# Optimization experiments

Measured on AMD Instinct MI355X. Metric: run time of the kernel, lower is better.

Reference implementation:

```python
import jax, jax.numpy as jnp
import numpy as np
from jax import lax

HEADS = 8
DIM_HEAD = 64
DIM = HEADS * DIM_HEAD  # 512


def _dwconv(x_nchw, w):
    # depthwise 3x3, stride 1, pad 1 (SAME), groups = channels
    return lax.conv_general_dilated(
        x_nchw, w, window_strides=(1, 1), padding='SAME',
        feature_group_count=x_nchw.shape[1],
        dimension_numbers=('NCHW', 'OIHW', 'NCHW'))


def setup_inputs() -> dict:
    key = jax.random.key(0)
    ks = jax.random.split(key, 9)
    b, h, w, c = 4, 256, 256, DIM
    s = 1.0 / np.sqrt(c)
    return {
        'x_in':    jax.random.normal(ks[0], (b, h, w, c), jnp.float32),
        'Wq':      jax.random.normal(ks[1], (c, DIM), jnp.float32) * s,
        'Wk':      jax.random.normal(ks[2], (c, DIM), jnp.float32) * s,
        'Wv':      jax.random.normal(ks[3], (c, DIM), jnp.float32) * s,
        'rescale': jnp.ones((HEADS, 1, 1), jnp.float32),
        'proj_w':  jax.random.normal(ks[4], (DIM, c), jnp.float32) * s,
        'proj_b':  jnp.zeros((c,), jnp.float32),
        'conv1_w': jax.random.normal(ks[5], (c, 1, 3, 3), jnp.float32) * (1.0 / 3.0),
        'conv2_w': jax.random.normal(ks[6], (c, 1, 3, 3), jnp.float32) * (1.0 / 3.0),
    }


def reference(x_in, Wq, Wk, Wv, rescale, proj_w, proj_b, conv1_w, conv2_w):
    b, h, w, c = x_in.shape
    n = h * w
    x = x_in.reshape(b, n, c)
    q_inp = x @ Wq  # [b, n, heads*d]
    k_inp = x @ Wk
    v_inp = x @ Wv

    def heads_dn(t):  # [b, n, heads*d] -> [b, heads, d, n]
        return t.reshape(b, n, HEADS, DIM_HEAD).transpose(0, 2, 3, 1)

    q = heads_dn(q_inp)
    k = heads_dn(k_inp)
    v = heads_dn(v_inp)

    # L2-normalize along token axis (F.normalize, eps=1e-12)
    qn = q / jnp.maximum(jnp.linalg.norm(q, axis=-1, keepdims=True), 1e-12)
    kn = k / jnp.maximum(jnp.linalg.norm(k, axis=-1, keepdims=True), 1e-12)

    # channel attention: [b, heads, d, d]
    attn = jnp.einsum('bhdn,bhen->bhde', kn, qn) * rescale
    attn = jax.nn.softmax(attn, axis=-1)
    xo = jnp.einsum('bhde,bhen->bhdn', attn, v)  # [b, heads, d, n]

    xo = xo.transpose(0, 3, 1, 2).reshape(b, n, HEADS * DIM_HEAD)
    out_c = (xo @ proj_w + proj_b).reshape(b, h, w, c)

    # depthwise conv positional embedding on v_inp
    vp = v_inp.reshape(b, h, w, c).transpose(0, 3, 1, 2)  # NCHW
    vp = _dwconv(vp, conv1_w)
    vp = jax.nn.gelu(vp, approximate=False)
    vp = _dwconv(vp, conv2_w)
    out_p = vp.transpose(0, 2, 3, 1)

    return out_c + out_p
```

## Files before the change

kernel.cpp:

```cpp
#include <hip/hip_runtime.h>
#include <math.h>

typedef unsigned short u16;
typedef unsigned int   u32;
typedef __attribute__((ext_vector_type(4))) float f32x4;
typedef __attribute__((ext_vector_type(8))) short bf16x8;
typedef __attribute__((ext_vector_type(8))) u16   u16x8;
typedef __attribute__((ext_vector_type(4))) u16   u16x4;

#define DEVI static __device__ __forceinline__

DEVI float bf2f(u16 a){ u32 u=((u32)a)<<16; float f; __builtin_memcpy(&f,&u,4); return f; }
DEVI u16 f2bf(float f){ u32 u; __builtin_memcpy(&u,&f,4); u=u+0x7fffu+((u>>16)&1u); return (u16)(u>>16); }

DEVI void gload16(const u16* src, u16* lds){
  __builtin_amdgcn_global_load_lds((const __attribute__((address_space(1))) u32*)src,
                                   (__attribute__((address_space(3))) u32*)lds, 16, 0, 0);
}

__global__ void k_wvt(const float* __restrict__ Wv, u16* __restrict__ WvT){
  int n = blockIdx.x;
  for (int k = threadIdx.x; k < 512; k += 256)
    WvT[(size_t)n*512 + k] = f2bf(Wv[(size_t)k*512 + n]);
}
__global__ void k_wrep(const float* __restrict__ w1, const float* __restrict__ w2, float* __restrict__ wt){
  int s = blockIdx.x/9, tap = blockIdx.x%9, c = threadIdx.x;
  const float* w = s ? w2 : w1;
  wt[(size_t)(s*9+tap)*512 + c] = w[(size_t)c*9 + tap];
}

__global__ __launch_bounds__(512) void k_gemm_v(const float* __restrict__ x, const u16* __restrict__ WvT,
                                                u16* __restrict__ v, u16* __restrict__ xbT){
  extern __shared__ __align__(16) u16 sm[];
  const int tid = threadIdx.x;
  const int l = tid & 63, w = tid >> 6;
  const long r0 = (long)blockIdx.x * 128;
  f32x4 acc[8][4] = {};

  const int arow = tid >> 2, ac = tid & 3;
  const float* xp = x + (r0 + arow)*512 + ac*8;
  f32x4 rAa, rAb;

  auto LOADA = [&](int kk){ rAa = *(const f32x4*)(xp + kk); rAb = *(const f32x4*)(xp + kk + 4); };
  auto WRITEA = [&](int buf){
    u16x8 o;
    o[0]=f2bf(rAa.x); o[1]=f2bf(rAa.y); o[2]=f2bf(rAa.z); o[3]=f2bf(rAa.w);
    o[4]=f2bf(rAb.x); o[5]=f2bf(rAb.y); o[6]=f2bf(rAb.z); o[7]=f2bf(rAb.w);
    *(u16x8*)&sm[buf*4096 + arow*32 + ((ac ^ ((arow>>1)&3))*8)] = o;
  };
  auto GLOADB = [&](int buf, int kk){
    #pragma unroll
    for (int i = 0; i < 4; ++i){
      int blkrow = w*64 + i*16;
      int r = blkrow + (l>>2);
      const u16* src = WvT + (size_t)r*512 + kk + (((l&3) ^ ((l>>3)&3))*8);
      gload16(src, &sm[8192 + buf*16384 + blkrow*32]);
    }
  };

  LOADA(0); WRITEA(0); LOADA(32); GLOADB(0, 0);
  __syncthreads();
  for (int t = 0; t < 16; ++t){
    const int cur = t & 1;
    if (t < 15){
      WRITEA(cur^1);
      if (t < 14) LOADA((t+2)*32);
      GLOADB(cur^1, (t+1)*32);
    }
    const u16* Al = sm + cur*4096;
    const u16* Bl = sm + 8192 + cur*16384;
    bf16x8 bfr[4];
    #pragma unroll
    for (int nf = 0; nf < 4; ++nf){
      int row = w*64 + nf*16 + (l&15);
      bfr[nf] = *(const bf16x8*)&Bl[row*32 + (((l>>4) ^ ((row>>1)&3))*8)];
    }
    #pragma unroll
    for (int mf = 0; mf < 8; ++mf){
      int row = mf*16 + (l&15);
      bf16x8 af = *(const bf16x8*)&Al[row*32 + (((l>>4) ^ ((row>>1)&3))*8)];
      #pragma unroll
      for (int nf = 0; nf < 4; ++nf)
        acc[mf][nf] = __builtin_amdgcn_mfma_f32_16x16x32_bf16(af, bfr[nf], acc[mf][nf], 0,0,0);
    }
    {
      int chloc = tid & 31, tg = tid >> 5;
      u16x8 o;
      #pragma unroll
      for (int j = 0; j < 8; ++j){
        int tok = tg*8 + j;
        o[j] = Al[tok*32 + (((chloc>>3) ^ ((tok>>1)&3))*8) + (chloc&7)];
      }
      *(u16x8*)(xbT + (size_t)(t*32 + chloc)*262144 + r0 + tg*8) = o;
    }
    __syncthreads();
  }
  #pragma unroll
  for (int mf = 0; mf < 8; ++mf)
    #pragma unroll
    for (int nf = 0; nf < 4; ++nf){
      int col = w*64 + nf*16 + (l&15);
      #pragma unroll
      for (int j = 0; j < 4; ++j){
        long row = r0 + mf*16 + (l>>4)*4 + j;
        v[(size_t)row*512 + col] = f2bf(acc[mf][nf][j]);
      }
    }
}

__global__ __launch_bounds__(1024, 4) void k_syrk(const u16* __restrict__ xbT, float* __restrict__ P){
  __shared__ __align__(16) u16 AL[256*64];
  __shared__ __align__(16) u16 BL[256*64];
  const int bid = blockIdx.x;
  const int cs = bid & 63, combo = (bid>>6)%3, b = bid/192;
  const int hA = (combo==2) ? 1 : 0;
  const int tid = threadIdx.x;
  const int l = tid & 63, w = tid>>6, wi = w>>2, wj = w&3;
  const long tokb0 = (long)b*65536 + (long)cs*1024;
  const u16* Bread = (combo==1) ? BL : AL;
  f32x4 acc[4][4] = {};
  for (int st = 0; st < 16; ++st){
    const long tokb = tokb0 + st*64;
    #pragma unroll
    for (int i = 0; i < 2; ++i){
      int blkrow = w*16 + i*8;
      int r = blkrow + (l>>3);
      const u16* src = xbT + (size_t)(hA*256 + r)*262144 + tokb + (((l&7) ^ ((l>>3)&7))*8);
      gload16(src, &AL[blkrow*64]);
    }
    if (combo == 1){
      #pragma unroll
      for (int i = 0; i < 2; ++i){
        int blkrow = w*16 + i*8;
        int r = blkrow + (l>>3);
        const u16* src = xbT + (size_t)(256 + r)*262144 + tokb + (((l&7) ^ ((l>>3)&7))*8);
        gload16(src, &BL[blkrow*64]);
      }
    }
    __syncthreads();
    #pragma unroll
    for (int ks = 0; ks < 2; ++ks){
      bf16x8 af[4], bfr[4];
      #pragma unroll
      for (int mf = 0; mf < 4; ++mf){
        int row = wi*64 + mf*16 + (l&15);
        af[mf] = *(const bf16x8*)&AL[row*64 + (((ks*4 + (l>>4)) ^ (row&7))*8)];
      }
      #pragma unroll
      for (int nf = 0; nf < 4; ++nf){
        int row = wj*64 + nf*16 + (l&15);
        bfr[nf] = *(const bf16x8*)&Bread[row*64 + (((ks*4 + (l>>4)) ^ (row&7))*8)];
      }
      #pragma unroll
      for (int mf = 0; mf < 4; ++mf)
        #pragma unroll
        for (int nf = 0; nf < 4; ++nf)
          acc[mf][nf] = __builtin_amdgcn_mfma_f32_16x16x32_bf16(af[mf], bfr[nf], acc[mf][nf], 0,0,0);
    }
    __syncthreads();
  }
  float* Pb = P + (size_t)bid*65536;
  #pragma unroll
  for (int mf = 0; mf < 4; ++mf)
    #pragma unroll
    for (int nf = 0; nf < 4; ++nf)
      #pragma unroll
      for (int j = 0; j < 4; ++j){
        int il = wi*64 + mf*16 + (l>>4)*4 + j;
        int jl = wj*64 + nf*16 + (l&15);
        Pb[il*256 + jl] = acc[mf][nf][j];
      }
}

__global__ void k_sred(const float* __restrict__ P, float* __restrict__ S){
  int bid = blockIdx.x;
  int il = bid & 255, combo = (bid>>8)%3, b = bid/768;
  int hi = (combo==2)?1:0, hj = (combo==0)?0:1;
  int jl = threadIdx.x;
  float s = 0.f;
  for (int cs = 0; cs < 64; ++cs)
    s += P[((size_t)(b*192 + combo*64 + cs))*65536 + il*256 + jl];
  int I = hi*256 + il, J = hj*256 + jl;
  S[((size_t)b*512 + I)*512 + J] = s;
  if (combo == 1) S[((size_t)b*512 + J)*512 + I] = s;
}

__global__ __launch_bounds__(256) void k_a1(const float* __restrict__ S, const float* __restrict__ Wq,
                                            const float* __restrict__ Wk, float* __restrict__ T, float* __restrict__ U){
  int bid = blockIdx.x;
  int b = bid>>6, rem = bid&63, which = rem>>5, rbase = (rem&31)*16;
  const float* W = which ? Wk : Wq;
  float* O = which ? U : T;
  int tid = threadIdx.x;
  int rg = tid>>6, c0 = (tid&63)*8;
  const float* Sr = S + (size_t)b*262144 + (size_t)(rbase + rg*4)*512;
  float acc[4][8] = {};
  for (int k = 0; k < 512; ++k){
    float s0 = Sr[k], s1 = Sr[512+k], s2 = Sr[1024+k], s3 = Sr[1536+k];
    f32x4 wa = *(const f32x4*)(W + (size_t)k*512 + c0);
    f32x4 wb = *(const f32x4*)(W + (size_t)k*512 + c0 + 4);
    #pragma unroll
    for (int j = 0; j < 4; ++j){
      acc[0][j]   += s0*wa[j]; acc[1][j]   += s1*wa[j]; acc[2][j]   += s2*wa[j]; acc[3][j]   += s3*wa[j];
      acc[0][4+j] += s0*wb[j]; acc[1][4+j] += s1*wb[j]; acc[2][4+j] += s2*wb[j]; acc[3][4+j] += s3*wb[j];
    }
  }
  float* Ob = O + (size_t)b*262144;
  #pragma unroll
  for (int i = 0; i < 4; ++i){
    f32x4 o0, o1;
    o0.x=acc[i][0]; o0.y=acc[i][1]; o0.z=acc[i][2]; o0.w=acc[i][3];
    o1.x=acc[i][4]; o1.y=acc[i][5]; o1.z=acc[i][6]; o1.w=acc[i][7];
    *(f32x4*)(Ob + (size_t)(rbase+rg*4+i)*512 + c0)     = o0;
    *(f32x4*)(Ob + (size_t)(rbase+rg*4+i)*512 + c0 + 4) = o1;
  }
}

__global__ void k_a2(const float* __restrict__ Wq, const float* __restrict__ Wk,
                     const float* __restrict__ T, const float* __restrict__ U,
                     float* __restrict__ G, float* __restrict__ q2, float* __restrict__ k2){
  int b = blockIdx.x>>3, h = blockIdx.x&7;
  int tid = threadIdx.x;
  int d0 = (tid>>4)*4, e0 = (tid&15)*4;
  const float* Tb = T + (size_t)b*262144;
  float acc[4][4] = {};
  for (int i = 0; i < 512; ++i){
    f32x4 wk = *(const f32x4*)(Wk + (size_t)i*512 + h*64 + d0);
    f32x4 tv = *(const f32x4*)(Tb + (size_t)i*512 + h*64 + e0);
    #pragma unroll
    for (int di = 0; di < 4; ++di)
      #pragma unroll
      for (int ej = 0; ej < 4; ++ej) acc[di][ej] += wk[di]*tv[ej];
  }
  float* Gb = G + ((size_t)(b*8+h))*4096;
  #pragma unroll
  for (int di = 0; di < 4; ++di)
    #pragma unroll
    for (int ej = 0; ej < 4; ++ej) Gb[(d0+di)*64 + e0+ej] = acc[di][ej];
  if (tid < 64){
    int e = tid; float a = 0.f;
    for (int j = 0; j < 512; ++j) a += Wq[(size_t)j*512 + h*64 + e] * Tb[(size_t)j*512 + h*64 + e];
    q2[b*512 + h*64 + e] = a;
  } else if (tid < 128){
    int d = tid - 64; float a = 0.f;
    const float* Ub = U + (size_t)b*262144;
    for (int j = 0; j < 512; ++j) a += Wk[(size_t)j*512 + h*64 + d] * Ub[(size_t)j*512 + h*64 + d];
    k2[b*512 + h*64 + d] = a;
  }
}

__global__ void k_a3(const float* __restrict__ G, const float* __restrict__ resc,
                     const float* __restrict__ q2, const float* __restrict__ k2, float* __restrict__ Aa){
  int b = blockIdx.x>>3, h = blockIdx.x&7;
  int d = threadIdx.x;
  const float* g = G + ((size_t)(b*8+h))*4096 + d*64;
  float kn = fmaxf(sqrtf(k2[b*512 + h*64 + d]), 1e-12f);
  float sc = resc[h] / kn;
  float m = -3.4e38f;
  for (int e = 0; e < 64; ++e){
    float qn = fmaxf(sqrtf(q2[b*512 + h*64 + e]), 1e-12f);
    m = fmaxf(m, g[e]*sc/qn);
  }
  float ssum = 0.f;
  for (int e = 0; e < 64; ++e){
    float qn = fmaxf(sqrtf(q2[b*512 + h*64 + e]), 1e-12f);
    ssum += expf(g[e]*sc/qn - m);
  }
  float inv = 1.0f/ssum;
  float* ao = Aa + ((size_t)(b*8+h))*4096 + d*64;
  for (int e = 0; e < 64; ++e){
    float qn = fmaxf(sqrtf(q2[b*512 + h*64 + e]), 1e-12f);
    ao[e] = expf(g[e]*sc/qn - m)*inv;
  }
}

__global__ void k_a4(const float* __restrict__ Aa, const float* __restrict__ pw, u16* __restrict__ MT){
  int bid = blockIdx.x;
  int jt = bid&3, h = (bid>>2)&7, b = bid>>5;
  int tid = threadIdx.x;
  int j = jt*128 + (tid&127), eh = tid>>7;
  const float* Ab = Aa + ((size_t)(b*8+h))*4096;
  float acc[32] = {};
  for (int d = 0; d < 64; ++d){
    float p = pw[(size_t)(h*64+d)*512 + j];
    const float* ar = Ab + d*64 + eh*32;
    #pragma unroll
    for (int q = 0; q < 8; ++q){
      f32x4 pa = *(const f32x4*)(ar + q*4);
      acc[q*4+0] += pa.x*p; acc[q*4+1] += pa.y*p; acc[q*4+2] += pa.z*p; acc[q*4+3] += pa.w*p;
    }
  }
  u16* mo = MT + (size_t)b*262144 + (size_t)j*512 + h*64 + eh*32;
  #pragma unroll
  for (int q = 0; q < 16; ++q){
    u32 pk = (u32)f2bf(acc[2*q]) | ((u32)f2bf(acc[2*q+1])<<16);
    *(u32*)&mo[2*q] = pk;
  }
}

__global__ __launch_bounds__(256) void k_conv_fused(const u16* __restrict__ v, const float* __restrict__ wt,
                                                    u16* __restrict__ cbuf){
  __shared__ float vtf[400*16];
  __shared__ float t1f[324*16];
  const int logical = (blockIdx.x & 7)*4096 + (blockIdx.x >> 3);
  const int g = logical & 31, tx = (logical>>5)&15, ty = (logical>>9)&15, b = logical>>13;
  const int c0 = g*16, oy0 = ty*16, ox0 = tx*16;
  const int tid = threadIdx.x;
  const int quad = tid & 3;

  for (int k = 0; k < 7; ++k){
    int q = tid + k*256; if (q >= 1600) break;
    int pos = q >> 2;
    int ly = pos / 20, lx = pos - ly*20;
    int gy = oy0 - 2 + ly, gx = ox0 - 2 + lx;
    f32x4 val = {};
    if (gy >= 0 && gy < 256 && gx >= 0 && gx < 256){
      u16x4 raw = *(const u16x4*)(v + ((size_t)(b*65536 + gy*256 + gx))*512 + c0 + quad*4);
      val.x = bf2f(raw[0]); val.y = bf2f(raw[1]); val.z = bf2f(raw[2]); val.w = bf2f(raw[3]);
    }
    *(f32x4*)&vtf[pos*16 + quad*4] = val;
  }

  f32x4 wq[9];
  #pragma unroll
  for (int tap = 0; tap < 9; ++tap)
    wq[tap] = *(const f32x4*)(wt + (size_t)tap*512 + c0 + quad*4);
  __syncthreads();

  for (int k = 0; k < 6; ++k){
    int q = tid + k*256; if (q >= 1296) break;
    int pos = q >> 2;
    int y1 = pos / 18, x1 = pos - y1*18;
    int gy1 = oy0 - 1 + y1, gx1 = ox0 - 1 + x1;
    bool inimg = (gy1 >= 0 && gy1 < 256 && gx1 >= 0 && gx1 < 256);
    const float* base = &vtf[(y1*20 + x1)*16 + quad*4];
    float acc[4] = {};
    #pragma unroll
    for (int tap = 0; tap < 9; ++tap){
      int dy = tap/3, dx = tap - dy*3;
      f32x4 vv = *(const f32x4*)(base + (dy*20 + dx)*16);
      #pragma unroll
      for (int j = 0; j < 4; ++j) acc[j] += vv[j]*wq[tap][j];
    }
    f32x4 o;
    #pragma unroll
    for (int j = 0; j < 4; ++j){
      float a = acc[j];
      float gl = a / (1.0f + __expf(-1.5957691216f*a*(1.0f + 0.044715f*a*a)));
      o[j] = inimg ? gl : 0.0f;
    }
    *(f32x4*)&t1f[pos*16 + quad*4] = o;
  }

  #pragma unroll
  for (int tap = 0; tap < 9; ++tap)
    wq[tap] = *(const f32x4*)(wt + (size_t)(9+tap)*512 + c0 + quad*4);
  __syncthreads();

  #pragma unroll
  for (int k = 0; k < 4; ++k){
    int q = tid + k*256;
    int pos = q >> 2;
    int y2 = pos >> 4, x2 = pos & 15;
    const float* base = &t1f[(y2*18 + x2)*16 + quad*4];
    float acc[4] = {};
    #pragma unroll
    for (int tap = 0; tap < 9; ++tap){
      int dy = tap/3, dx = tap - dy*3;
      f32x4 tt = *(const f32x4*)(base + (dy*18 + dx)*16);
      #pragma unroll
      for (int j = 0; j < 4; ++j) acc[j] += tt[j]*wq[tap][j];
    }
    u16x4 o;
    #pragma unroll
    for (int j = 0; j < 4; ++j) o[j] = f2bf(acc[j]);
    size_t tok = (size_t)b*65536 + (size_t)(oy0+y2)*256 + (ox0+x2);
    *(u16x4*)(cbuf + tok*512 + c0 + quad*4) = o;
  }
}

__global__ __launch_bounds__(512, 2) void k_gemm_out(const u16* __restrict__ v, const u16* __restrict__ MT,
                                                     const float* __restrict__ proj_b, const u16* __restrict__ cbuf,
                                                     float* __restrict__ out){
  extern __shared__ __align__(16) u16 sm[];
  const int tid = threadIdx.x;
  const int l = tid & 63, w = tid >> 6;
  const int wr = w >> 2, wc = w & 3;
  const int bid = blockIdx.x;
  const int wg = (bid & 7)*256 + (bid >> 3);
  const long r0 = (long)(wg >> 1) * 256;
  const int  c0b = (wg & 1) * 256;
  const int  b = (int)(r0 >> 16);
  const u16* Mb = MT + (size_t)b*262144;
  f32x4 acc[8][4] = {};

  auto STAGE = [&](int buf, int k0){
    u16* Ab = sm + buf*16384;
    u16* Bb = sm + 32768 + buf*16384;
    #pragma unroll
    for (int i = 0; i < 4; ++i){
      int blkrow = w*32 + i*8;
      int r = blkrow + (l>>3);
      gload16(v + (size_t)(r0 + r)*512 + k0 + (((l&7) ^ (r&7))*8), Ab + blkrow*64);
    }
    #pragma unroll
    for (int i = 0; i < 4; ++i){
      int blkrow = w*32 + i*8;
      int r = blkrow + (l>>3);
      gload16(Mb + (size_t)(c0b + r)*512 + k0 + (((l&7) ^ (r&7))*8), Bb + blkrow*64);
    }
  };

  STAGE(0, 0);
  __syncthreads();
  for (int t = 0; t < 8; ++t){
    const int cur = t & 1;
    if (t < 7) STAGE(cur^1, (t+1)*64);
    const u16* Al = sm + cur*16384;
    const u16* Bl = sm + 32768 + cur*16384;
    #pragma unroll
    for (int ks = 0; ks < 2; ++ks){
      bf16x8 bfr[4];
      #pragma unroll
      for (int nf = 0; nf < 4; ++nf){
        int row = wc*64 + nf*16 + (l&15);
        bfr[nf] = *(const bf16x8*)&Bl[row*64 + (((ks*4 + (l>>4)) ^ (row&7))*8)];
      }
      #pragma unroll
      for (int mf = 0; mf < 8; ++mf){
        int row = wr*128 + mf*16 + (l&15);
        bf16x8 af = *(const bf16x8*)&Al[row*64 + (((ks*4 + (l>>4)) ^ (row&7))*8)];
        #pragma unroll
        for (int nf = 0; nf < 4; ++nf)
          acc[mf][nf] = __builtin_amdgcn_mfma_f32_16x16x32_bf16(af, bfr[nf], acc[mf][nf], 0,0,0);
      }
    }
    __syncthreads();
  }
  #pragma unroll
  for (int mf = 0; mf < 8; ++mf)
    #pragma unroll
    for (int nf = 0; nf < 4; ++nf){
      int col = c0b + wc*64 + nf*16 + (l&15);
      float pb = proj_b[col];
      #pragma unroll
      for (int j = 0; j < 4; ++j){
        long row = r0 + wr*128 + mf*16 + (l>>4)*4 + j;
        out[(size_t)row*512 + col] = acc[mf][nf][j] + pb + bf2f(cbuf[(size_t)row*512 + col]);
      }
    }
}

extern "C" void kernel_launch(void* const* d_in, const int* in_sizes, int n_in,
                              void* d_out, int out_size, void* d_ws, size_t ws_size,
                              hipStream_t stream){
  const float* x   = (const float*)d_in[0];
  const float* Wq  = (const float*)d_in[1];
  const float* Wk  = (const float*)d_in[2];
  const float* Wv  = (const float*)d_in[3];
  const float* rsc = (const float*)d_in[4];
  const float* pw  = (const float*)d_in[5];
  const float* pb  = (const float*)d_in[6];
  const float* w1  = (const float*)d_in[7];
  const float* w2  = (const float*)d_in[8];
  float* out = (float*)d_out;
  char* ws = (char*)d_ws;

  const size_t MB256 = 268435456;
  u16*   v    = (u16*)ws;
  u16*   xbT  = (u16*)(ws + MB256);
  u16*   cbuf = xbT;
  char*  sm0  = ws + 2*MB256;
  float* P    = (float*)d_out;

  float* S   = (float*)(sm0);
  float* Tm  = (float*)(sm0 + 4194304);
  float* Um  = (float*)(sm0 + 8388608);
  float* G   = (float*)(sm0 + 12582912);
  float* Aa  = (float*)(sm0 + 13107200);
  float* q2  = (float*)(sm0 + 13631488);
  float* k2  = (float*)(sm0 + 13639680);
  u16*   MT  = (u16*)  (sm0 + 13647872);
  u16*   WvT = (u16*)  (sm0 + 15745024);
  float* wt  = (float*)(sm0 + 16269312);

  k_wvt <<<512, 256, 0, stream>>>(Wv, WvT);
  k_wrep<<<18, 512, 0, stream>>>(w1, w2, wt);
  k_gemm_v<<<2048, 512, 81920, stream>>>(x, WvT, v, xbT);
  k_syrk<<<768, 1024, 0, stream>>>(xbT, P);
  k_sred<<<3072, 256, 0, stream>>>(P, S);
  k_a1<<<256, 256, 0, stream>>>(S, Wq, Wk, Tm, Um);
  k_a2<<<32, 256, 0, stream>>>(Wq, Wk, Tm, Um, G, q2, k2);
  k_a3<<<32, 64, 0, stream>>>(G, rsc, q2, k2, Aa);
  k_a4<<<128, 256, 0, stream>>>(Aa, pw, MT);
  k_conv_fused<<<32768, 256, 0, stream>>>(v, wt, cbuf);
  k_gemm_out<<<2048, 512, 131072, stream>>>(v, MT, pb, cbuf, out);
}
```

Before: 1.513 ms.

## Double-buffer syrk tiles with larger warp tiles; register-block depthwise conv outputs

The syrk kernel now uses 512 threads with each wave computing a 128x64 tile, and it double-buffers the LDS stages so the next token chunk loads while the current one feeds MFMA. This is meant to hide global-to-LDS latency and cut per-FLOP LDS traffic. The depthwise conv stages now have each thread compute four adjacent x outputs from a sliding window of six loaded columns, which reduces LDS reads per output. The cost is 128KB of dynamic LDS and more accumulator registers in syrk, which limits occupancy to one block per CU.

Result: no change. 1.518 ms (+0.3%).

```diff
diff --git a/kernel.cpp b/kernel.cpp
--- a/kernel.cpp
+++ b/kernel.cpp
@@ -108,65 +108,70 @@
     }
 }
 
-__global__ __launch_bounds__(1024, 4) void k_syrk(const u16* __restrict__ xbT, float* __restrict__ P){
-  __shared__ __align__(16) u16 AL[256*64];
-  __shared__ __align__(16) u16 BL[256*64];
+__global__ __launch_bounds__(512) void k_syrk(const u16* __restrict__ xbT, float* __restrict__ P){
+  extern __shared__ __align__(16) u16 sm[];
   const int bid = blockIdx.x;
   const int cs = bid & 63, combo = (bid>>6)%3, b = bid/192;
   const int hA = (combo==2) ? 1 : 0;
   const int tid = threadIdx.x;
-  const int l = tid & 63, w = tid>>6, wi = w>>2, wj = w&3;
+  const int l = tid & 63, w = tid >> 6;
+  const int wi = w >> 2, wj = w & 3;
   const long tokb0 = (long)b*65536 + (long)cs*1024;
-  const u16* Bread = (combo==1) ? BL : AL;
-  f32x4 acc[4][4] = {};
-  for (int st = 0; st < 16; ++st){
-    const long tokb = tokb0 + st*64;
-    #pragma unroll
-    for (int i = 0; i < 2; ++i){
-      int blkrow = w*16 + i*8;
+  f32x4 acc[8][4] = {};
+
+  auto STAGE = [&](int buf, long tokb){
+    u16* Ab = sm + buf*16384;
+    #pragma unroll
+    for (int i = 0; i < 4; ++i){
+      int blkrow = w*32 + i*8;
       int r = blkrow + (l>>3);
-      const u16* src = xbT + (size_t)(hA*256 + r)*262144 + tokb + (((l&7) ^ ((l>>3)&7))*8);
-      gload16(src, &AL[blkrow*64]);
+      gload16(xbT + (size_t)(hA*256 + r)*262144 + tokb + (((l&7) ^ ((l>>3)&7))*8), Ab + blkrow*64);
     }
     if (combo == 1){
-      #pragma unroll
-      for (int i = 0; i < 2; ++i){
-        int blkrow = w*16 + i*8;
+      u16* Bb = sm + 32768 + buf*16384;
+      #pragma unroll
+      for (int i = 0; i < 4; ++i){
+        int blkrow = w*32 + i*8;
         int r = blkrow + (l>>3);
-        const u16* src = xbT + (size_t)(256 + r)*262144 + tokb + (((l&7) ^ ((l>>3)&7))*8);
-        gload16(src, &BL[blkrow*64]);
-      }
-    }
-    __syncthreads();
+        gload16(xbT + (size_t)(256 + r)*262144 + tokb + (((l&7) ^ ((l>>3)&7))*8), Bb + blkrow*64);
+      }
+    }
+  };
+
+  STAGE(0, tokb0);
+  __syncthreads();
+  for (int t = 0; t < 16; ++t){
+    const int cur = t & 1;
+    if (t < 15) STAGE(cur^1, tokb0 + (t+1)*64);
+    const u16* Al = sm + cur*16384;
+    const u16* Bl = (combo==1) ? (sm + 32768 + cur*16384) : Al;
     #pragma unroll
     for (int ks = 0; ks < 2; ++ks){
-      bf16x8 af[4], bfr[4];
-      #pragma unroll
-      for (int mf = 0; mf < 4; ++mf){
-        int row = wi*64 + mf*16 + (l&15);
-        af[mf] = *(const bf16x8*)&AL[row*64 + (((ks*4 + (l>>4)) ^ (row&7))*8)];
-      }
+      bf16x8 bfr[4];
       #pragma unroll
       for (int nf = 0; nf < 4; ++nf){
         int row = wj*64 + nf*16 + (l&15);
-        bfr[nf] = *(const bf16x8*)&Bread[row*64 + (((ks*4 + (l>>4)) ^ (row&7))*8)];
-      }
-      #pragma unroll
-      for (int mf = 0; mf < 4; ++mf)
+        bfr[nf] = *(const bf16x8*)&Bl[row*64 + (((ks*4 + (l>>4)) ^ (row&7))*8)];
+      }
+      #pragma unroll
+      for (int mf = 0; mf < 8; ++mf){
+        int row = wi*128 + mf*16 + (l&15);
+        bf16x8 af = *(const bf16x8*)&Al[row*64 + (((ks*4 + (l>>4)) ^ (row&7))*8)];
         #pragma unroll
         for (int nf = 0; nf < 4; ++nf)
-          acc[mf][nf] = __builtin_amdgcn_mfma_f32_16x16x32_bf16(af[mf], bfr[nf], acc[mf][nf], 0,0,0);
+          acc[mf][nf] = __builtin_amdgcn_mfma_f32_16x16x32_bf16(af, bfr[nf], acc[mf][nf], 0,0,0);
+      }
     }
     __syncthreads();
   }
   float* Pb = P + (size_t)bid*65536;
   #pragma unroll
-  for (int mf = 0; mf < 4; ++mf)
+  for (int mf = 0; mf < 8; ++mf)
     #pragma unroll
     for (int nf = 0; nf < 4; ++nf)
       #pragma unroll
       for (int j = 0; j < 4; ++j){
-        int il = wi*64 + mf*16 + (l>>4)*4 + j;
+        int il = wi*128 + mf*16 + (l>>4)*4 + j;
         int jl = wj*64 + nf*16 + (l&15);
         Pb[il*256 + jl] = acc[mf][nf][j];
       }
@@ -327,29 +332,47 @@
     wq[tap] = *(const f32x4*)(wt + (size_t)tap*512 + c0 + quad*4);
   __syncthreads();
 
-  for (int k = 0; k < 6; ++k){
-    int q = tid + k*256; if (q >= 1296) break;
-    int pos = q >> 2;
-    int y1 = pos / 18, x1 = pos - y1*18;
-    int gy1 = oy0 - 1 + y1, gx1 = ox0 - 1 + x1;
-    bool inimg = (gy1 >= 0 && gy1 < 256 && gx1 >= 0 && gx1 < 256);
-    const float* base = &vtf[(y1*20 + x1)*16 + quad*4];
-    float acc[4] = {};
-    #pragma unroll
-    for (int tap = 0; tap < 9; ++tap){
-      int dy = tap/3, dx = tap - dy*3;
-      f32x4 vv = *(const f32x4*)(base + (dy*20 + dx)*16);
-      #pragma unroll
-      for (int j = 0; j < 4; ++j) acc[j] += vv[j]*wq[tap][j];
-    }
-    f32x4 o;
-    #pragma unroll
-    for (int j = 0; j < 4; ++j){
-      float a = acc[j];
-      float gl = a / (1.0f + __expf(-1.5957691216f*a*(1.0f + 0.044715f*a*a)));
-      o[j] = inimg ? gl : 0.0f;
-    }
-    *(f32x4*)&t1f[pos*16 + quad*4] = o;
+  for (int task = tid; task < 1440; task += 256){
+    int tq = task & 3;
+    int rest = task >> 2;
+    if (rest >= 90) break;
+    int chunk = rest % 5, y1 = rest / 5;
+    int x1b = chunk*4;
+    float acc[4][4] = {{0.f}};
+    #pragma unroll
+    for (int cc = 0; cc < 6; ++cc){
+      int lx = x1b + cc; lx = lx > 19 ? 19 : lx;
+      #pragma unroll
+      for (int dy = 0; dy < 3; ++dy){
+        f32x4 s = *(const f32x4*)&vtf[((y1+dy)*20 + lx)*16 + tq*4];
+        #pragma unroll
+        for (int ox = 0; ox < 4; ++ox){
+          int dx = cc - ox;
+          if (dx >= 0 && dx < 3){
+            f32x4 w = wq[dy*3 + dx];
+            #pragma unroll
+            for (int j = 0; j < 4; ++j) acc[ox][j] += s[j]*w[j];
+          }
+        }
+      }
+    }
+    int gy1 = oy0 - 1 + y1;
+    #pragma unroll
+    for (int ox = 0; ox < 4; ++ox){
+      int x1 = x1b + ox;
+      if (x1 < 18){
+        int gx1 = ox0 - 1 + x1;
+        bool inimg = (gy1 >= 0 && gy1 < 256 && gx1 >= 0 && gx1 < 256);
+        f32x4 o;
+        #pragma unroll
+        for (int j = 0; j < 4; ++j){
+          float a = acc[ox][j];
+          float gl = a / (1.0f + __expf(-1.5957691216f*a*(1.0f + 0.044715f*a*a)));
+          o[j] = inimg ? gl : 0.0f;
+        }
+        *(f32x4*)&t1f[(y1*18 + x1)*16 + tq*4] = o;
+      }
+    }
   }
 
   #pragma unroll
@@ -357,25 +380,36 @@
     wq[tap] = *(const f32x4*)(wt + (size_t)(9+tap)*512 + c0 + quad*4);
   __syncthreads();
 
-  #pragma unroll
-  for (int k = 0; k < 4; ++k){
-    int q = tid + k*256;
-    int pos = q >> 2;
-    int y2 = pos >> 4, x2 = pos & 15;
-    const float* base = &t1f[(y2*18 + x2)*16 + quad*4];
-    float acc[4] = {};
-    #pragma unroll
-    for (int tap = 0; tap < 9; ++tap){
-      int dy = tap/3, dx = tap - dy*3;
-      f32x4 tt = *(const f32x4*)(base + (dy*18 + dx)*16);
-      #pragma unroll
-      for (int j = 0; j < 4; ++j) acc[j] += tt[j]*wq[tap][j];
-    }
-    u16x4 o;
-    #pragma unroll
-    for (int j = 0; j < 4; ++j) o[j] = f2bf(acc[j]);
-    size_t tok = (size_t)b*65536 + (size_t)(oy0+y2)*256 + (ox0+x2);
-    *(u16x4*)(cbuf + tok*512 + c0 + quad*4) = o;
+  {
+    int rest = tid >> 2;
+    int chunk = rest & 3, y2 = rest >> 2;
+    int x2b = chunk*4;
+    float acc[4][4] = {{0.f}};
+    #pragma unroll
+    for (int cc = 0; cc < 6; ++cc){
+      int lx = x2b + cc;
+      #pragma unroll
+      for (int dy = 0; dy < 3; ++dy){
+        f32x4 s = *(const f32x4*)&t1f[((y2+dy)*18 + lx)*16 + quad*4];
+        #pragma unroll
+        for (int ox = 0; ox < 4; ++ox){
+          int dx = cc - ox;
+          if (dx >= 0 && dx < 3){
+            f32x4 w = wq[dy*3 + dx];
+            #pragma unroll
+            for (int j = 0; j < 4; ++j) acc[ox][j] += s[j]*w[j];
+          }
+        }
+      }
+    }
+    #pragma unroll
+    for (int ox = 0; ox < 4; ++ox){
+      u16x4 o;
+      #pragma unroll
+      for (int j = 0; j < 4; ++j) o[j] = f2bf(acc[ox][j]);
+      size_t tok = (size_t)b*65536 + (size_t)(oy0+y2)*256 + (ox0 + x2b + ox);
+      *(u16x4*)(cbuf + tok*512 + c0 + quad*4) = o;
+    }
   }
 }
 
@@ -487,7 +521,7 @@
   k_wvt <<<512, 256, 0, stream>>>(Wv, WvT);
   k_wrep<<<18, 512, 0, stream>>>(w1, w2, wt);
   k_gemm_v<<<2048, 512, 81920, stream>>>(x, WvT, v, xbT);
-  k_syrk<<<768, 1024, 0, stream>>>(xbT, P);
+  k_syrk<<<768, 512, 131072, stream>>>(xbT, P);
   k_sred<<<3072, 256, 0, stream>>>(P, S);
   k_a1<<<256, 256, 0, stream>>>(S, Wq, Wk, Tm, Um);
   k_a2<<<32, 256, 0, stream>>>(Wq, Wk, Tm, Um, G, q2, k2);
```
